# Performance work log

Measured on AMD Instinct MI355X. Metric: run time of the kernel, lower is better.

Reference implementation:

```python
import jax, jax.numpy as jnp
import numpy as np

V, E, A, H, L, T = 30000, 512, 512, 512, 2, 20
U, P, B = 10000, 10000, 32


def setup_inputs():
    key = jax.random.key(0)
    ks = jax.random.split(key, 25)
    s = 0.05
    f = lambda k, shp: jax.random.normal(k, shp, dtype=jnp.float32) * s
    return {
        "user": jax.random.randint(ks[0], (B,), 0, U),
        "product": jax.random.randint(ks[1], (B,), 0, P),
        "rating": jax.random.randint(ks[2], (B,), 0, 10),
        "trg": jax.random.randint(ks[3], (B, T), 0, V),
        "trg_lengths": jax.random.randint(ks[4], (B,), 1, T + 1),
        "embed": f(ks[5], (V, E)),
        "user_w": f(ks[6], (U, A)),
        "product_w": f(ks[7], (P, A)),
        "rating_w": f(ks[8], (10, A)),
        "enc_w": f(ks[9], (H * L, 3 * A)),
        "enc_b": f(ks[10], (H * L,)),
        "w_ih0": f(ks[11], (3 * H, E + H)),
        "w_hh0": f(ks[12], (3 * H, H)),
        "b_ih0": f(ks[13], (3 * H,)),
        "b_hh0": f(ks[14], (3 * H,)),
        "w_ih1": f(ks[15], (3 * H, H)),
        "w_hh1": f(ks[16], (3 * H, H)),
        "b_ih1": f(ks[17], (3 * H,)),
        "b_hh1": f(ks[18], (3 * H,)),
        "key_w": f(ks[19], (H, A)),
        "query_w": f(ks[20], (H, H)),
        "energy_w": f(ks[21], (1, H)),
        "ctx_w": f(ks[22], (H, H + A)),
        "ctx_b": f(ks[23], (H,)),
        "gen_w": f(ks[24], (V, H)),
    }


def _gru_cell(x, h, w_ih, w_hh, b_ih, b_hh):
    # torch GRU cell; gate order r, z, n
    gi = x @ w_ih.T + b_ih
    gh = h @ w_hh.T + b_hh
    ir, iz, inn = jnp.split(gi, 3, axis=-1)
    hr, hz, hn = jnp.split(gh, 3, axis=-1)
    r = jax.nn.sigmoid(ir + hr)
    z = jax.nn.sigmoid(iz + hz)
    n = jnp.tanh(inn + r * hn)
    return (1.0 - z) * n + z * h


def reference(user, product, rating, trg, trg_lengths, embed, user_w, product_w,
              rating_w, enc_w, enc_b, w_ih0, w_hh0, b_ih0, b_hh0, w_ih1, w_hh1,
              b_ih1, b_hh1, key_w, query_w, energy_w, ctx_w, ctx_b, gen_w):
    attr_cat = jnp.concatenate([user_w[user], product_w[product], rating_w[rating]], axis=-1)  # [B, 3A]
    attr_final = jax.nn.leaky_relu(attr_cat @ enc_w.T + enc_b, 0.01).reshape(-1, L, H)
    attr_final = jnp.transpose(attr_final, (1, 0, 2))  # [L, B, H]
    encoder_attr = attr_cat.reshape(-1, 3, A)          # [B, 3, A]
    proj_key = encoder_attr @ key_w.T                  # [B, 3, H]
    trg_embed = embed[trg]                             # [B, T, E]
    bos = jnp.broadcast_to(embed[1], (trg.shape[0], 1, E))  # start token id 1
    prev = jnp.concatenate([bos, trg_embed[:, : T - 1]], axis=1)  # teacher forcing
    xs = jnp.transpose(prev, (1, 0, 2))                # [T, B, E]

    def step(carry, x):
        h0, h1, ctx = carry
        rnn_in = jnp.concatenate([x, ctx], axis=-1)    # [B, E+H]
        h0n = _gru_cell(rnn_in, h0, w_ih0, w_hh0, b_ih0, b_hh0)
        h1n = _gru_cell(h0n, h1, w_ih1, w_hh1, b_ih1, b_hh1)
        q = h1n @ query_w.T                            # [B, H]
        scores = jnp.tanh(q[:, None, :] + proj_key) @ energy_w[0]  # [B, 3]
        alphas = jax.nn.softmax(scores, axis=-1)
        context = jnp.einsum('bk,bka->ba', alphas, encoder_attr)   # [B, A]
        ctxn = jnp.tanh(jnp.concatenate([h1n, context], axis=-1) @ ctx_w.T + ctx_b)
        logp = jax.nn.log_softmax(ctxn @ gen_w.T, axis=-1)          # [B, V]
        return (h0n, h1n, ctxn), logp

    init = (attr_final[0], attr_final[1], attr_final[-1])
    _, out = jax.lax.scan(step, init, xs)              # [T, B, V]
    return jnp.transpose(out, (1, 0, 2))               # [B, T, V]
```

## Files before the change

kernel.cpp:

```cpp
#include <hip/hip_runtime.h>
#include <math.h>

#define BB 32
#define TT 20
#define VV 30000

typedef short short8 __attribute__((ext_vector_type(8)));
typedef unsigned short ushort8 __attribute__((ext_vector_type(8)));
typedef float floatx4 __attribute__((ext_vector_type(4)));

__device__ __forceinline__ float dot4(float4 a, float4 b) {
  return a.x*b.x + a.y*b.y + a.z*b.z + a.w*b.w;
}

__device__ __forceinline__ unsigned short f2bf(float f) {
  unsigned int u = __builtin_bit_cast(unsigned int, f);
  u = u + 0x7fffu + ((u >> 16) & 1u);
  return (unsigned short)(u >> 16);
}

__global__ __launch_bounds__(256) void k_cvt(const float* __restrict__ src,
                                             unsigned short* __restrict__ dst, int n8)
{
  int i = blockIdx.x*256 + threadIdx.x;
  if (i >= n8) return;
  const float4* s = ((const float4*)src) + (size_t)i*2;
  float4 a = s[0], b = s[1];
  ushort8 v;
  v[0]=f2bf(a.x); v[1]=f2bf(a.y); v[2]=f2bf(a.z); v[3]=f2bf(a.w);
  v[4]=f2bf(b.x); v[5]=f2bf(b.y); v[6]=f2bf(b.z); v[7]=f2bf(b.w);
  ((ushort8*)dst)[i] = v;
}

__global__ __launch_bounds__(256) void k_prep(const int* __restrict__ user, const int* __restrict__ product,
    const int* __restrict__ rating, const int* __restrict__ trg,
    const float* __restrict__ embed, const float* __restrict__ user_w,
    const float* __restrict__ product_w, const float* __restrict__ rating_w,
    float* __restrict__ attr_cat, float* __restrict__ xs)
{
  int i = blockIdx.x*256 + threadIdx.x;
  if (i < BB*1536) {
    int b = i / 1536, j = i - b*1536;
    float v;
    if (j < 512)       v = user_w[(size_t)user[b]*512 + j];
    else if (j < 1024) v = product_w[(size_t)product[b]*512 + (j-512)];
    else               v = rating_w[(size_t)rating[b]*512 + (j-1024)];
    attr_cat[i] = v;
  }
  int i2 = i - BB*1536;
  if (i2 >= 0 && i2 < TT*BB*512) {
    int t = i2 >> 14;
    int r = i2 & 16383;
    int b = r >> 9, e = r & 511;
    int tok = (t == 0) ? 1 : trg[b*TT + (t-1)];
    xs[i2] = embed[(size_t)tok*512 + e];
  }
}

__global__ __launch_bounds__(256) void k_enc(const float* __restrict__ attr_cat, const float* __restrict__ enc_w,
    const float* __restrict__ enc_b, float* __restrict__ h0, float* __restrict__ h1, float* __restrict__ ctx0)
{
  int i = blockIdx.x*256 + threadIdx.x;
  int b = i & 31, j = i >> 5;
  const float4* a = (const float4*)(attr_cat + b*1536);
  const float4* w = (const float4*)(enc_w + (size_t)j*1536);
  float acc = 0.f;
  #pragma unroll 8
  for (int k = 0; k < 384; k++) acc += dot4(a[k], w[k]);
  acc += enc_b[j];
  float v = acc > 0.f ? acc : 0.01f*acc;
  if (j < 512) h0[b*512 + j] = v;
  else { h1[b*512 + (j-512)] = v; ctx0[b*512 + (j-512)] = v; }
}

__global__ __launch_bounds__(256) void k_key(const float* __restrict__ attr_cat, const float* __restrict__ key_w,
    float* __restrict__ proj_key)
{
  int i = blockIdx.x*256 + threadIdx.x;
  int b = i & 31, j = i >> 5;
  int k3 = j >> 9, h = j & 511;
  const float4* a = (const float4*)(attr_cat + b*1536 + k3*512);
  const float4* w = (const float4*)(key_w + (size_t)h*512);
  float acc = 0.f;
  #pragma unroll 8
  for (int k = 0; k < 128; k++) acc += dot4(a[k], w[k]);
  proj_key[(b*3 + k3)*512 + h] = acc;
}

__global__ __launch_bounds__(256) void k_gx(const float* __restrict__ xs, const float* __restrict__ w_ih0,
    const float* __restrict__ b_ih0, float* __restrict__ gx)
{
  int i = blockIdx.x*256 + threadIdx.x;
  int m = i / 1536, g = i - m*1536;
  const float4* xv = (const float4*)(xs + (size_t)m*512);
  const float4* wv = (const float4*)(w_ih0 + (size_t)g*1024);
  float a = b_ih0[g];
  #pragma unroll 4
  for (int k = 0; k < 128; k++) a += dot4(xv[k], wv[k]);
  gx[i] = a;
}

__global__ __launch_bounds__(256) void k_gru2(
    const float* __restrict__ x, const float* __restrict__ h_in,
    const float* __restrict__ wi, int wi_stride,
    const float* __restrict__ wh,
    const float* __restrict__ gx, const float* __restrict__ bi,
    const float* __restrict__ bh, float* __restrict__ h_out)
{
  int tid = threadIdx.x;
  int ks = tid & 7;
  int b  = tid >> 3;
  int h  = blockIdx.x;
  const float4* xv = (const float4*)(x + b*512 + ks*64);
  const float4* hv = (const float4*)(h_in + b*512 + ks*64);
  float acc[6];
  #pragma unroll
  for (int g = 0; g < 3; g++) {
    const float4* wiv = (const float4*)(wi + (size_t)(g*512 + h)*wi_stride + ks*64);
    const float4* whv = (const float4*)(wh + (size_t)(g*512 + h)*512 + ks*64);
    float ai = 0.f, ah = 0.f;
    #pragma unroll
    for (int k = 0; k < 16; k++) { ai += dot4(xv[k], wiv[k]); ah += dot4(hv[k], whv[k]); }
    acc[g] = ai; acc[3+g] = ah;
  }
  #pragma unroll
  for (int d = 1; d < 8; d <<= 1) {
    #pragma unroll
    for (int j = 0; j < 6; j++) acc[j] += __shfl_xor(acc[j], d);
  }
  if (ks == 0) {
    float ir = acc[0], iz = acc[1], inn = acc[2];
    float hr = acc[3], hz = acc[4], hn = acc[5];
    if (gx) { ir += gx[b*1536 + h]; iz += gx[b*1536 + 512 + h]; inn += gx[b*1536 + 1024 + h]; }
    else    { ir += bi[h]; iz += bi[512+h]; inn += bi[1024+h]; }
    hr += bh[h]; hz += bh[512+h]; hn += bh[1024+h];
    float r = 1.f/(1.f + expf(-(ir+hr)));
    float z = 1.f/(1.f + expf(-(iz+hz)));
    float n = tanhf(inn + r*hn);
    h_out[b*512+h] = (1.f - z)*n + z*h_in[b*512+h];
  }
}

__global__ __launch_bounds__(256) void k_q(const float* __restrict__ h1n, const float* __restrict__ query_w,
    float* __restrict__ q)
{
  int tid = threadIdx.x; int ks = tid & 7; int b = tid >> 3; int h = blockIdx.x;
  const float4* xv = (const float4*)(h1n + b*512 + ks*64);
  const float4* wv = (const float4*)(query_w + (size_t)h*512 + ks*64);
  float a = 0.f;
  #pragma unroll
  for (int k = 0; k < 16; k++) a += dot4(xv[k], wv[k]);
  #pragma unroll
  for (int d = 1; d < 8; d <<= 1) a += __shfl_xor(a, d);
  if (ks == 0) q[b*512+h] = a;
}

__global__ __launch_bounds__(256) void k_attn_sc(const float* __restrict__ q, const float* __restrict__ proj_key,
    const float* __restrict__ attr_cat, const float* __restrict__ energy_w, float* __restrict__ context)
{
  __shared__ float red3[768];
  __shared__ float al[3];
  int b = blockIdx.x, tid = threadIdx.x;
  float s0 = 0.f, s1 = 0.f, s2 = 0.f;
  for (int h = tid; h < 512; h += 256) {
    float e = energy_w[h], qq = q[b*512 + h];
    s0 += tanhf(qq + proj_key[(b*3+0)*512 + h]) * e;
    s1 += tanhf(qq + proj_key[(b*3+1)*512 + h]) * e;
    s2 += tanhf(qq + proj_key[(b*3+2)*512 + h]) * e;
  }
  red3[tid] = s0; red3[256+tid] = s1; red3[512+tid] = s2;
  __syncthreads();
  for (int st = 128; st > 0; st >>= 1) {
    if (tid < st) {
      red3[tid]     += red3[tid+st];
      red3[256+tid] += red3[256+tid+st];
      red3[512+tid] += red3[512+tid+st];
    }
    __syncthreads();
  }
  if (tid == 0) {
    float sc0 = red3[0], sc1 = red3[256], sc2 = red3[512];
    float mx = fmaxf(sc0, fmaxf(sc1, sc2));
    float e0 = expf(sc0-mx), e1 = expf(sc1-mx), e2 = expf(sc2-mx);
    float inv = 1.f/(e0+e1+e2);
    al[0] = e0*inv; al[1] = e1*inv; al[2] = e2*inv;
  }
  __syncthreads();
  for (int a = tid; a < 512; a += 256)
    context[b*512 + a] = al[0]*attr_cat[b*1536 + a] + al[1]*attr_cat[b*1536 + 512 + a]
                       + al[2]*attr_cat[b*1536 + 1024 + a];
}

__global__ __launch_bounds__(256) void k_ctx(const float* __restrict__ h1n, const float* __restrict__ context,
    const float* __restrict__ ctx_w, const float* __restrict__ ctx_b, float* __restrict__ out)
{
  int tid = threadIdx.x; int ks = tid & 7; int b = tid >> 3; int h = blockIdx.x;
  const float4* xv = (const float4*)(h1n + b*512 + ks*64);
  const float4* cv = (const float4*)(context + b*512 + ks*64);
  const float4* w1 = (const float4*)(ctx_w + (size_t)h*1024 + ks*64);
  const float4* w2 = (const float4*)(ctx_w + (size_t)h*1024 + 512 + ks*64);
  float a = 0.f;
  #pragma unroll
  for (int k = 0; k < 16; k++) { a += dot4(xv[k], w1[k]); a += dot4(cv[k], w2[k]); }
  #pragma unroll
  for (int d = 1; d < 8; d <<= 1) a += __shfl_xor(a, d);
  if (ks == 0) out[b*512+h] = tanhf(a + ctx_b[h]);
}

__global__ __launch_bounds__(256) void k_gen(const unsigned short* __restrict__ Abf,
    const unsigned short* __restrict__ Bbf, float* __restrict__ out)
{
  __shared__ unsigned short As[128*64];
  __shared__ unsigned short Bs[128*64];
  int tid = threadIdx.x;
  int ntile = blockIdx.x, mtile = blockIdx.y;
  int lane = tid & 63, wave = tid >> 6;
  int quad = lane >> 4, l15 = lane & 15;
  int wm = (wave >> 1) * 64, wn = (wave & 1) * 64;
  int m0 = mtile * 128, n0 = ntile * 128;
  floatx4 acc[4][4] = {};
  for (int kt = 0; kt < 8; kt++) {
    __syncthreads();
    #pragma unroll
    for (int c = 0; c < 4; c++) {
      int f = c*256 + tid;
      int row = f >> 3, k8 = (f & 7) * 8;
      ((short8*)As)[f] = *(const short8*)(Abf + (size_t)(m0 + row)*512 + kt*64 + k8);
      int vr = n0 + row; if (vr > VV-1) vr = VV-1;
      ((short8*)Bs)[f] = *(const short8*)(Bbf + (size_t)vr*512 + kt*64 + k8);
    }
    __syncthreads();
    #pragma unroll
    for (int ks = 0; ks < 2; ks++) {
      short8 af[4], bfr[4];
      #pragma unroll
      for (int i = 0; i < 4; i++)
        af[i] = *(const short8*)&As[(wm + i*16 + l15)*64 + ks*32 + quad*8];
      #pragma unroll
      for (int j = 0; j < 4; j++)
        bfr[j] = *(const short8*)&Bs[(wn + j*16 + l15)*64 + ks*32 + quad*8];
      #pragma unroll
      for (int i = 0; i < 4; i++)
        #pragma unroll
        for (int j = 0; j < 4; j++)
          acc[i][j] = __builtin_amdgcn_mfma_f32_16x16x32_bf16(af[i], bfr[j], acc[i][j], 0, 0, 0);
    }
  }
  #pragma unroll
  for (int i = 0; i < 4; i++) {
    int mbase = m0 + wm + i*16 + quad*4;
    #pragma unroll
    for (int j = 0; j < 4; j++) {
      int v = n0 + wn + j*16 + l15;
      if (v < VV) {
        #pragma unroll
        for (int r = 0; r < 4; r++) {
          int m = mbase + r;
          out[(size_t)((m & 31)*TT + (m >> 5))*VV + v] = acc[i][j][r];
        }
      }
    }
  }
}

__global__ __launch_bounds__(256) void k_logsm(float* __restrict__ out)
{
  __shared__ float red[256];
  int row = blockIdx.x, tid = threadIdx.x;
  float* p = out + (size_t)row*VV;
  float4* pv = (float4*)p;
  float m = -1e30f;
  for (int i = tid; i < VV/4; i += 256) {
    float4 v = pv[i];
    m = fmaxf(m, fmaxf(fmaxf(v.x, v.y), fmaxf(v.z, v.w)));
  }
  red[tid] = m; __syncthreads();
  for (int st = 128; st > 0; st >>= 1) { if (tid < st) red[tid] = fmaxf(red[tid], red[tid+st]); __syncthreads(); }
  m = red[0]; __syncthreads();
  float s = 0.f;
  for (int i = tid; i < VV/4; i += 256) {
    float4 v = pv[i];
    s += __expf(v.x-m) + __expf(v.y-m) + __expf(v.z-m) + __expf(v.w-m);
  }
  red[tid] = s; __syncthreads();
  for (int st = 128; st > 0; st >>= 1) { if (tid < st) red[tid] += red[tid+st]; __syncthreads(); }
  float lse = m + logf(red[0]);
  for (int i = tid; i < VV/4; i += 256) {
    float4 v = pv[i];
    v.x -= lse; v.y -= lse; v.z -= lse; v.w -= lse;
    pv[i] = v;
  }
}

extern "C" void kernel_launch(void* const* d_in, const int* in_sizes, int n_in,
                              void* d_out, int out_size, void* d_ws, size_t ws_size,
                              hipStream_t stream)
{
  const int*   user      = (const int*)d_in[0];
  const int*   product   = (const int*)d_in[1];
  const int*   rating    = (const int*)d_in[2];
  const int*   trg       = (const int*)d_in[3];
  const float* embed     = (const float*)d_in[5];
  const float* user_w    = (const float*)d_in[6];
  const float* product_w = (const float*)d_in[7];
  const float* rating_w  = (const float*)d_in[8];
  const float* enc_w     = (const float*)d_in[9];
  const float* enc_b     = (const float*)d_in[10];
  const float* w_ih0     = (const float*)d_in[11];
  const float* w_hh0     = (const float*)d_in[12];
  const float* b_ih0     = (const float*)d_in[13];
  const float* b_hh0     = (const float*)d_in[14];
  const float* w_ih1     = (const float*)d_in[15];
  const float* w_hh1     = (const float*)d_in[16];
  const float* b_ih1     = (const float*)d_in[17];
  const float* b_hh1     = (const float*)d_in[18];
  const float* key_w     = (const float*)d_in[19];
  const float* query_w   = (const float*)d_in[20];
  const float* energy_w  = (const float*)d_in[21];
  const float* ctx_w     = (const float*)d_in[22];
  const float* ctx_b     = (const float*)d_in[23];
  const float* gen_w     = (const float*)d_in[24];
  float* out = (float*)d_out;

  float* ws       = (float*)d_ws;
  float* attr_cat = ws;
  float* xs       = attr_cat + 49152;
  float* proj_key = xs + 327680;
  float* h0buf    = proj_key + 49152;
  float* h1buf    = h0buf + 32768;
  float* ctx_all  = h1buf + 32768;
  float* gx_all   = ctx_all + 344064;
  float* qbuf     = gx_all + 983040;
  float* context  = qbuf + 16384;
  unsigned short* genw_bf = (unsigned short*)(context + 16384);
  unsigned short* act_bf  = genw_bf + 15360000;

  k_cvt<<<7500, 256, 0, stream>>>(gen_w, genw_bf, 1920000);
  k_prep<<<1472, 256, 0, stream>>>(user, product, rating, trg, embed, user_w, product_w, rating_w,
                                   attr_cat, xs);
  k_enc<<<128, 256, 0, stream>>>(attr_cat, enc_w, enc_b, h0buf, h1buf, ctx_all);
  k_key<<<192, 256, 0, stream>>>(attr_cat, key_w, proj_key);
  k_gx<<<3840, 256, 0, stream>>>(xs, w_ih0, b_ih0, gx_all);

  for (int t = 0; t < TT; t++) {
    const float* ctxt = ctx_all + t*BB*512;
    float* h0_in  = h0buf + (t & 1)*BB*512;
    float* h0_out = h0buf + ((t+1) & 1)*BB*512;
    float* h1_in  = h1buf + (t & 1)*BB*512;
    float* h1_out = h1buf + ((t+1) & 1)*BB*512;
    k_gru2<<<512, 256, 0, stream>>>(ctxt, h0_in, w_ih0 + 512, 1024, w_hh0,
                                    gx_all + (size_t)t*BB*1536, nullptr, b_hh0, h0_out);
    k_gru2<<<512, 256, 0, stream>>>(h0_out, h1_in, w_ih1, 512, w_hh1,
                                    nullptr, b_ih1, b_hh1, h1_out);
    k_q<<<512, 256, 0, stream>>>(h1_out, query_w, qbuf);
    k_attn_sc<<<32, 256, 0, stream>>>(qbuf, proj_key, attr_cat, energy_w, context);
    k_ctx<<<512, 256, 0, stream>>>(h1_out, context, ctx_w, ctx_b, ctx_all + (t+1)*BB*512);
  }

  k_cvt<<<160, 256, 0, stream>>>(ctx_all + BB*512, act_bf, 40960);
  dim3 ggrid(235, 5);
  k_gen<<<ggrid, 256, 0, stream>>>(act_bf, genw_bf, out);
  k_logsm<<<640, 256, 0, stream>>>(out);
}
```

Baseline: 3.800 ms.

## Fuse recurrent loop into persistent kernel with grid barrier; MFMA input GEMM

Replaces the 100 per-step kernel launches of the recurrent loop with a single persistent kernel of 256 blocks. The blocks are synchronised between stages by an atomic grid barrier, and the attention and context stage runs in only 32 blocks. The layer-0 input projection now runs as a bf16 MFMA GEMM over bf16 embeddings and bf16 weights instead of a scalar fp32 kernel. This aims to remove launch overhead and speed up the precompute, but it depends on all blocks being co-resident, leaves most blocks idle during the attention stage, and lowers the precision of the input projection.

```diff
diff --git a/kernel.cpp b/kernel.cpp
--- a/kernel.cpp
+++ b/kernel.cpp
@@ -4,6 +4,7 @@
 #define BB 32
 #define TT 20
 #define VV 30000
+#define NBLK 256
 
 typedef short short8 __attribute__((ext_vector_type(8)));
 typedef unsigned short ushort8 __attribute__((ext_vector_type(8)));
@@ -17,6 +18,11 @@
   unsigned int u = __builtin_bit_cast(unsigned int, f);
   u = u + 0x7fffu + ((u >> 16) & 1u);
   return (unsigned short)(u >> 16);
+}
+
+__global__ void k_zero(unsigned* __restrict__ bar)
+{
+  if (threadIdx.x < 2) bar[threadIdx.x] = 0u;
 }
 
 __global__ __launch_bounds__(256) void k_cvt(const float* __restrict__ src,
@@ -36,7 +42,7 @@
     const int* __restrict__ rating, const int* __restrict__ trg,
     const float* __restrict__ embed, const float* __restrict__ user_w,
     const float* __restrict__ product_w, const float* __restrict__ rating_w,
-    float* __restrict__ attr_cat, float* __restrict__ xs)
+    float* __restrict__ attr_cat, unsigned short* __restrict__ xs_bf)
 {
   int i = blockIdx.x*256 + threadIdx.x;
   if (i < BB*1536) {
@@ -53,7 +59,7 @@
     int r = i2 & 16383;
     int b = r >> 9, e = r & 511;
     int tok = (t == 0) ? 1 : trg[b*TT + (t-1)];
-    xs[i2] = embed[(size_t)tok*512 + e];
+    xs_bf[i2] = f2bf(embed[(size_t)tok*512 + e]);
   }
 }
 
@@ -87,124 +93,233 @@
   proj_key[(b*3 + k3)*512 + h] = acc;
 }
 
-__global__ __launch_bounds__(256) void k_gx(const float* __restrict__ xs, const float* __restrict__ w_ih0,
-    const float* __restrict__ b_ih0, float* __restrict__ gx)
-{
-  int i = blockIdx.x*256 + threadIdx.x;
-  int m = i / 1536, g = i - m*1536;
-  const float4* xv = (const float4*)(xs + (size_t)m*512);
-  const float4* wv = (const float4*)(w_ih0 + (size_t)g*1024);
-  float a = b_ih0[g];
-  #pragma unroll 4
-  for (int k = 0; k < 128; k++) a += dot4(xv[k], wv[k]);
-  gx[i] = a;
-}
-
-__global__ __launch_bounds__(256) void k_gru2(
-    const float* __restrict__ x, const float* __restrict__ h_in,
-    const float* __restrict__ wi, int wi_stride,
-    const float* __restrict__ wh,
-    const float* __restrict__ gx, const float* __restrict__ bi,
-    const float* __restrict__ bh, float* __restrict__ h_out)
-{
+__global__ __launch_bounds__(256) void k_gx_mfma(const unsigned short* __restrict__ Abf,
+    const unsigned short* __restrict__ Bbf, const float* __restrict__ bias, float* __restrict__ out)
+{
+  __shared__ unsigned short As[128*64];
+  __shared__ unsigned short Bs[128*64];
   int tid = threadIdx.x;
+  int ntile = blockIdx.x, mtile = blockIdx.y;
+  int lane = tid & 63, wave = tid >> 6;
+  int quad = lane >> 4, l15 = lane & 15;
+  int wm = (wave >> 1) * 64, wn = (wave & 1) * 64;
+  int m0 = mtile * 128, n0 = ntile * 128;
+  floatx4 acc[4][4] = {};
+  for (int kt = 0; kt < 8; kt++) {
+    __syncthreads();
+    #pragma unroll
+    for (int c = 0; c < 4; c++) {
+      int f = c*256 + tid;
+      int row = f >> 3, k8 = (f & 7) * 8;
+      ((short8*)As)[f] = *(const short8*)(Abf + (size_t)(m0 + row)*512 + kt*64 + k8);
+      ((short8*)Bs)[f] = *(const short8*)(Bbf + (size_t)(n0 + row)*1024 + kt*64 + k8);
+    }
+    __syncthreads();
+    #pragma unroll
+    for (int ks = 0; ks < 2; ks++) {
+      short8 af[4], bfr[4];
+      #pragma unroll
+      for (int i = 0; i < 4; i++)
+        af[i] = *(const short8*)&As[(wm + i*16 + l15)*64 + ks*32 + quad*8];
+      #pragma unroll
+      for (int j = 0; j < 4; j++)
+        bfr[j] = *(const short8*)&Bs[(wn + j*16 + l15)*64 + ks*32 + quad*8];
+      #pragma unroll
+      for (int i = 0; i < 4; i++)
+        #pragma unroll
+        for (int j = 0; j < 4; j++)
+          acc[i][j] = __builtin_amdgcn_mfma_f32_16x16x32_bf16(af[i], bfr[j], acc[i][j], 0, 0, 0);
+    }
+  }
+  #pragma unroll
+  for (int i = 0; i < 4; i++) {
+    int mbase = m0 + wm + i*16 + quad*4;
+    #pragma unroll
+    for (int j = 0; j < 4; j++) {
+      int n = n0 + wn + j*16 + l15;
+      float bv = bias[n];
+      #pragma unroll
+      for (int r = 0; r < 4; r++)
+        out[(size_t)(mbase + r)*1536 + n] = acc[i][j][r] + bv;
+    }
+  }
+}
+
+__device__ __forceinline__ void gsync(unsigned* bar)
+{
+  __syncthreads();
+  if (threadIdx.x == 0) {
+    __threadfence();
+    unsigned g = atomicOr(bar + 1, 0u);
+    if (atomicAdd(bar, 1u) == NBLK - 1u) {
+      atomicAnd(bar, 0u);
+      __threadfence();
+      atomicAdd(bar + 1, 1u);
+    } else {
+      while (atomicOr(bar + 1, 0u) == g)
+        __builtin_amdgcn_s_sleep(4);
+    }
+    __threadfence();
+  }
+  __syncthreads();
+}
+
+__global__ __launch_bounds__(256) void k_rec(
+    const float* __restrict__ gx_all, const float* __restrict__ wih0c,
+    const float* __restrict__ whh0, const float* __restrict__ bhh0,
+    const float* __restrict__ wih1, const float* __restrict__ bih1,
+    const float* __restrict__ whh1, const float* __restrict__ bhh1,
+    const float* __restrict__ query_w, const float* __restrict__ energy_w,
+    const float* __restrict__ ctx_w, const float* __restrict__ ctx_b,
+    const float* __restrict__ proj_key, const float* __restrict__ attr_cat,
+    float* __restrict__ h0buf, float* __restrict__ h1buf, float* __restrict__ ctx_all,
+    unsigned* __restrict__ bar)
+{
+  __shared__ float h1s[512];
+  __shared__ float q[512];
+  __shared__ float cv[512];
+  __shared__ float red3[768];
+  __shared__ float al[3];
+  int tid = threadIdx.x, blk = blockIdx.x;
   int ks = tid & 7;
   int b  = tid >> 3;
-  int h  = blockIdx.x;
-  const float4* xv = (const float4*)(x + b*512 + ks*64);
-  const float4* hv = (const float4*)(h_in + b*512 + ks*64);
-  float acc[6];
-  #pragma unroll
-  for (int g = 0; g < 3; g++) {
-    const float4* wiv = (const float4*)(wi + (size_t)(g*512 + h)*wi_stride + ks*64);
-    const float4* whv = (const float4*)(wh + (size_t)(g*512 + h)*512 + ks*64);
-    float ai = 0.f, ah = 0.f;
-    #pragma unroll
-    for (int k = 0; k < 16; k++) { ai += dot4(xv[k], wiv[k]); ah += dot4(hv[k], whv[k]); }
-    acc[g] = ai; acc[3+g] = ah;
-  }
-  #pragma unroll
-  for (int d = 1; d < 8; d <<= 1) {
-    #pragma unroll
-    for (int j = 0; j < 6; j++) acc[j] += __shfl_xor(acc[j], d);
-  }
-  if (ks == 0) {
-    float ir = acc[0], iz = acc[1], inn = acc[2];
-    float hr = acc[3], hz = acc[4], hn = acc[5];
-    if (gx) { ir += gx[b*1536 + h]; iz += gx[b*1536 + 512 + h]; inn += gx[b*1536 + 1024 + h]; }
-    else    { ir += bi[h]; iz += bi[512+h]; inn += bi[1024+h]; }
-    hr += bh[h]; hz += bh[512+h]; hn += bh[1024+h];
-    float r = 1.f/(1.f + expf(-(ir+hr)));
-    float z = 1.f/(1.f + expf(-(iz+hz)));
-    float n = tanhf(inn + r*hn);
-    h_out[b*512+h] = (1.f - z)*n + z*h_in[b*512+h];
-  }
-}
-
-__global__ __launch_bounds__(256) void k_q(const float* __restrict__ h1n, const float* __restrict__ query_w,
-    float* __restrict__ q)
-{
-  int tid = threadIdx.x; int ks = tid & 7; int b = tid >> 3; int h = blockIdx.x;
-  const float4* xv = (const float4*)(h1n + b*512 + ks*64);
-  const float4* wv = (const float4*)(query_w + (size_t)h*512 + ks*64);
-  float a = 0.f;
-  #pragma unroll
-  for (int k = 0; k < 16; k++) a += dot4(xv[k], wv[k]);
-  #pragma unroll
-  for (int d = 1; d < 8; d <<= 1) a += __shfl_xor(a, d);
-  if (ks == 0) q[b*512+h] = a;
-}
-
-__global__ __launch_bounds__(256) void k_attn_sc(const float* __restrict__ q, const float* __restrict__ proj_key,
-    const float* __restrict__ attr_cat, const float* __restrict__ energy_w, float* __restrict__ context)
-{
-  __shared__ float red3[768];
-  __shared__ float al[3];
-  int b = blockIdx.x, tid = threadIdx.x;
-  float s0 = 0.f, s1 = 0.f, s2 = 0.f;
-  for (int h = tid; h < 512; h += 256) {
-    float e = energy_w[h], qq = q[b*512 + h];
-    s0 += tanhf(qq + proj_key[(b*3+0)*512 + h]) * e;
-    s1 += tanhf(qq + proj_key[(b*3+1)*512 + h]) * e;
-    s2 += tanhf(qq + proj_key[(b*3+2)*512 + h]) * e;
-  }
-  red3[tid] = s0; red3[256+tid] = s1; red3[512+tid] = s2;
-  __syncthreads();
-  for (int st = 128; st > 0; st >>= 1) {
-    if (tid < st) {
-      red3[tid]     += red3[tid+st];
-      red3[256+tid] += red3[256+tid+st];
-      red3[512+tid] += red3[512+tid+st];
-    }
-    __syncthreads();
-  }
-  if (tid == 0) {
-    float sc0 = red3[0], sc1 = red3[256], sc2 = red3[512];
-    float mx = fmaxf(sc0, fmaxf(sc1, sc2));
-    float e0 = expf(sc0-mx), e1 = expf(sc1-mx), e2 = expf(sc2-mx);
-    float inv = 1.f/(e0+e1+e2);
-    al[0] = e0*inv; al[1] = e1*inv; al[2] = e2*inv;
-  }
-  __syncthreads();
-  for (int a = tid; a < 512; a += 256)
-    context[b*512 + a] = al[0]*attr_cat[b*1536 + a] + al[1]*attr_cat[b*1536 + 512 + a]
-                       + al[2]*attr_cat[b*1536 + 1024 + a];
-}
-
-__global__ __launch_bounds__(256) void k_ctx(const float* __restrict__ h1n, const float* __restrict__ context,
-    const float* __restrict__ ctx_w, const float* __restrict__ ctx_b, float* __restrict__ out)
-{
-  int tid = threadIdx.x; int ks = tid & 7; int b = tid >> 3; int h = blockIdx.x;
-  const float4* xv = (const float4*)(h1n + b*512 + ks*64);
-  const float4* cv = (const float4*)(context + b*512 + ks*64);
-  const float4* w1 = (const float4*)(ctx_w + (size_t)h*1024 + ks*64);
-  const float4* w2 = (const float4*)(ctx_w + (size_t)h*1024 + 512 + ks*64);
-  float a = 0.f;
-  #pragma unroll
-  for (int k = 0; k < 16; k++) { a += dot4(xv[k], w1[k]); a += dot4(cv[k], w2[k]); }
-  #pragma unroll
-  for (int d = 1; d < 8; d <<= 1) a += __shfl_xor(a, d);
-  if (ks == 0) out[b*512+h] = tanhf(a + ctx_b[h]);
+
+  for (int t = 0; t < TT; t++) {
+    const float* ctx_t = ctx_all + t*BB*512;
+    const float* h0_in = h0buf + (t & 1)*BB*512;
+    float*       h0_out= h0buf + ((t+1) & 1)*BB*512;
+    const float* h1_in = h1buf + (t & 1)*BB*512;
+    float*       h1_out= h1buf + ((t+1) & 1)*BB*512;
+
+    {
+      const float4* xv = (const float4*)(ctx_t + b*512 + ks*64);
+      const float4* hv = (const float4*)(h0_in + b*512 + ks*64);
+      for (int hh = 0; hh < 2; hh++) {
+        int h = blk*2 + hh;
+        float acc[6];
+        #pragma unroll
+        for (int g = 0; g < 3; g++) {
+          const float4* wiv = (const float4*)(wih0c + (size_t)(g*512 + h)*1024 + ks*64);
+          const float4* whv = (const float4*)(whh0 + (size_t)(g*512 + h)*512 + ks*64);
+          float ai = 0.f, ah = 0.f;
+          #pragma unroll
+          for (int k = 0; k < 16; k++) { ai += dot4(xv[k], wiv[k]); ah += dot4(hv[k], whv[k]); }
+          acc[g] = ai; acc[3+g] = ah;
+        }
+        #pragma unroll
+        for (int d = 1; d < 8; d <<= 1) {
+          #pragma unroll
+          for (int j = 0; j < 6; j++) acc[j] += __shfl_xor(acc[j], d);
+        }
+        if (ks == 0) {
+          const float* gxrow = gx_all + (size_t)t*BB*1536;
+          float ir = acc[0] + gxrow[b*1536 + h];
+          float iz = acc[1] + gxrow[b*1536 + 512 + h];
+          float inn= acc[2] + gxrow[b*1536 + 1024 + h];
+          float hr = acc[3] + bhh0[h];
+          float hz = acc[4] + bhh0[512+h];
+          float hn = acc[5] + bhh0[1024+h];
+          float r = 1.f/(1.f + expf(-(ir+hr)));
+          float z = 1.f/(1.f + expf(-(iz+hz)));
+          float n = tanhf(inn + r*hn);
+          h0_out[b*512+h] = (1.f - z)*n + z*h0_in[b*512+h];
+        }
+      }
+    }
+    gsync(bar);
+
+    {
+      const float4* xv = (const float4*)(h0_out + b*512 + ks*64);
+      const float4* hv = (const float4*)(h1_in + b*512 + ks*64);
+      for (int hh = 0; hh < 2; hh++) {
+        int h = blk*2 + hh;
+        float acc[6];
+        #pragma unroll
+        for (int g = 0; g < 3; g++) {
+          const float4* wiv = (const float4*)(wih1 + (size_t)(g*512 + h)*512 + ks*64);
+          const float4* whv = (const float4*)(whh1 + (size_t)(g*512 + h)*512 + ks*64);
+          float ai = 0.f, ah = 0.f;
+          #pragma unroll
+          for (int k = 0; k < 16; k++) { ai += dot4(xv[k], wiv[k]); ah += dot4(hv[k], whv[k]); }
+          acc[g] = ai; acc[3+g] = ah;
+        }
+        #pragma unroll
+        for (int d = 1; d < 8; d <<= 1) {
+          #pragma unroll
+          for (int j = 0; j < 6; j++) acc[j] += __shfl_xor(acc[j], d);
+        }
+        if (ks == 0) {
+          float ir = acc[0] + bih1[h];
+          float iz = acc[1] + bih1[512+h];
+          float inn= acc[2] + bih1[1024+h];
+          float hr = acc[3] + bhh1[h];
+          float hz = acc[4] + bhh1[512+h];
+          float hn = acc[5] + bhh1[1024+h];
+          float r = 1.f/(1.f + expf(-(ir+hr)));
+          float z = 1.f/(1.f + expf(-(iz+hz)));
+          float n = tanhf(inn + r*hn);
+          h1_out[b*512+h] = (1.f - z)*n + z*h1_in[b*512+h];
+        }
+      }
+    }
+    gsync(bar);
+
+    if (blk < BB) {
+      int bb = blk;
+      for (int h = tid; h < 512; h += 256) h1s[h] = h1_out[bb*512 + h];
+      __syncthreads();
+      const float4* xv = (const float4*)h1s;
+      for (int h = tid; h < 512; h += 256) {
+        const float4* w = (const float4*)(query_w + (size_t)h*512);
+        float a = 0.f;
+        #pragma unroll 8
+        for (int k = 0; k < 128; k++) a += dot4(xv[k], w[k]);
+        q[h] = a;
+      }
+      __syncthreads();
+      float s0 = 0.f, s1 = 0.f, s2 = 0.f;
+      for (int h = tid; h < 512; h += 256) {
+        float e = energy_w[h], qq = q[h];
+        s0 += tanhf(qq + proj_key[(bb*3+0)*512 + h]) * e;
+        s1 += tanhf(qq + proj_key[(bb*3+1)*512 + h]) * e;
+        s2 += tanhf(qq + proj_key[(bb*3+2)*512 + h]) * e;
+      }
+      red3[tid] = s0; red3[256+tid] = s1; red3[512+tid] = s2;
+      __syncthreads();
+      for (int st = 128; st > 0; st >>= 1) {
+        if (tid < st) {
+          red3[tid]     += red3[tid+st];
+          red3[256+tid] += red3[256+tid+st];
+          red3[512+tid] += red3[512+tid+st];
+        }
+        __syncthreads();
+      }
+      if (tid == 0) {
+        float sc0 = red3[0], sc1 = red3[256], sc2 = red3[512];
+        float mx = fmaxf(sc0, fmaxf(sc1, sc2));
+        float e0 = expf(sc0-mx), e1 = expf(sc1-mx), e2 = expf(sc2-mx);
+        float inv = 1.f/(e0+e1+e2);
+        al[0] = e0*inv; al[1] = e1*inv; al[2] = e2*inv;
+      }
+      __syncthreads();
+      for (int a = tid; a < 512; a += 256)
+        cv[a] = al[0]*attr_cat[bb*1536 + a] + al[1]*attr_cat[bb*1536 + 512 + a]
+              + al[2]*attr_cat[bb*1536 + 1024 + a];
+      __syncthreads();
+      const float4* cvv = (const float4*)cv;
+      float* ctx_next = ctx_all + (t+1)*BB*512;
+      for (int h = tid; h < 512; h += 256) {
+        const float4* w1 = (const float4*)(ctx_w + (size_t)h*1024);
+        const float4* w2 = w1 + 128;
+        float a = ctx_b[h];
+        #pragma unroll 8
+        for (int k = 0; k < 128; k++) { a += dot4(xv[k], w1[k]); a += dot4(cvv[k], w2[k]); }
+        ctx_next[bb*512 + h] = tanhf(a);
+      }
+      __syncthreads();
+    }
+    gsync(bar);
+  }
 }
 
 __global__ __launch_bounds__(256) void k_gen(const unsigned short* __restrict__ Abf,
@@ -324,38 +439,32 @@
 
   float* ws       = (float*)d_ws;
   float* attr_cat = ws;
-  float* xs       = attr_cat + 49152;
-  float* proj_key = xs + 327680;
+  float* proj_key = attr_cat + 49152;
   float* h0buf    = proj_key + 49152;
   float* h1buf    = h0buf + 32768;
   float* ctx_all  = h1buf + 32768;
   float* gx_all   = ctx_all + 344064;
-  float* qbuf     = gx_all + 983040;
-  float* context  = qbuf + 16384;
-  unsigned short* genw_bf = (unsigned short*)(context + 16384);
+  unsigned* bar   = (unsigned*)(gx_all + 983040);
+  unsigned short* xs_bf   = (unsigned short*)(bar + 8);
+  unsigned short* wih0_bf = xs_bf + 327680;
+  unsigned short* genw_bf = wih0_bf + 1572864;
   unsigned short* act_bf  = genw_bf + 15360000;
 
+  k_zero<<<1, 64, 0, stream>>>(bar);
   k_cvt<<<7500, 256, 0, stream>>>(gen_w, genw_bf, 1920000);
+  k_cvt<<<768, 256, 0, stream>>>(w_ih0, wih0_bf, 196608);
   k_prep<<<1472, 256, 0, stream>>>(user, product, rating, trg, embed, user_w, product_w, rating_w,
-                                   attr_cat, xs);
+                                   attr_cat, xs_bf);
   k_enc<<<128, 256, 0, stream>>>(attr_cat, enc_w, enc_b, h0buf, h1buf, ctx_all);
   k_key<<<192, 256, 0, stream>>>(attr_cat, key_w, proj_key);
-  k_gx<<<3840, 256, 0, stream>>>(xs, w_ih0, b_ih0, gx_all);
-
-  for (int t = 0; t < TT; t++) {
-    const float* ctxt = ctx_all + t*BB*512;
-    float* h0_in  = h0buf + (t & 1)*BB*512;
-    float* h0_out = h0buf + ((t+1) & 1)*BB*512;
-    float* h1_in  = h1buf + (t & 1)*BB*512;
-    float* h1_out = h1buf + ((t+1) & 1)*BB*512;
-    k_gru2<<<512, 256, 0, stream>>>(ctxt, h0_in, w_ih0 + 512, 1024, w_hh0,
-                                    gx_all + (size_t)t*BB*1536, nullptr, b_hh0, h0_out);
-    k_gru2<<<512, 256, 0, stream>>>(h0_out, h1_in, w_ih1, 512, w_hh1,
-                                    nullptr, b_ih1, b_hh1, h1_out);
-    k_q<<<512, 256, 0, stream>>>(h1_out, query_w, qbuf);
-    k_attn_sc<<<32, 256, 0, stream>>>(qbuf, proj_key, attr_cat, energy_w, context);
-    k_ctx<<<512, 256, 0, stream>>>(h1_out, context, ctx_w, ctx_b, ctx_all + (t+1)*BB*512);
-  }
+  dim3 ggx(12, 5);
+  k_gx_mfma<<<ggx, 256, 0, stream>>>(xs_bf, wih0_bf, b_ih0, gx_all);
+
+  k_rec<<<NBLK, 256, 0, stream>>>(gx_all, w_ih0 + 512, w_hh0, b_hh0,
+                                  w_ih1, b_ih1, w_hh1, b_hh1,
+                                  query_w, energy_w, ctx_w, ctx_b,
+                                  proj_key, attr_cat,
+                                  h0buf, h1buf, ctx_all, bar);
 
   k_cvt<<<160, 256, 0, stream>>>(ctx_all + BB*512, act_bf, 40960);
   dim3 ggrid(235, 5);
```

After: 5.917 ms. +55.7%, slower.
